# Kernel optimization log

Hardware: AMD Instinct MI355X
Metric: run time of the kernel (lower is better)

Reference implementation:

```python
import jax, jax.numpy as jnp
import numpy as np

B, D, K, A = 32768, 256, 1024, 32
MIN_LOG_STD, MAX_LOG_STD = -20.0, 2.0


def setup_inputs() -> dict:
    key = jax.random.key(0)
    ks = jax.random.split(key, 9)
    return {
        "obs": jax.random.normal(ks[0], (B, D), dtype=jnp.float32),
        "mean_C": jax.random.normal(ks[1], (K, D), dtype=jnp.float32),
        "mean_sigma": jnp.abs(jax.random.normal(ks[2], (K,), dtype=jnp.float32)) + 0.1,
        "mean_w": jax.random.normal(ks[3], (A, K), dtype=jnp.float32),
        "mean_b": jax.random.normal(ks[4], (A,), dtype=jnp.float32),
        "std_C": jax.random.normal(ks[5], (K, D), dtype=jnp.float32),
        "std_sigma": jnp.abs(jax.random.normal(ks[6], (K,), dtype=jnp.float32)) + 0.1,
        "std_w": jax.random.normal(ks[7], (A, K), dtype=jnp.float32),
        "std_b": jax.random.normal(ks[8], (A,), dtype=jnp.float32),
    }


def _rbf(x, C, sigma_sq, w, b):
    # r[b,k] = sum_d (x[b,d] - C[k,d])^2, expanded to avoid a [B,K,D] intermediate
    x2 = jnp.sum(x * x, axis=-1, keepdims=True)           # [B,1]
    c2 = jnp.sum(C * C, axis=-1)[None, :]                  # [1,K]
    r = x2 - 2.0 * (x @ C.T) + c2                          # [B,K]
    phi = jnp.exp(-r / (2.0 * jnp.abs(sigma_sq)[None, :]))  # [B,K]
    return phi @ w.T + b[None, :]                          # [B,A]


def reference(obs, mean_C, mean_sigma, mean_w, mean_b,
              std_C, std_sigma, std_w, std_b):
    action_mean = _rbf(obs, mean_C, mean_sigma, mean_w, mean_b)
    std_raw = _rbf(obs, std_C, std_sigma, std_w, std_b)
    action_std = jnp.exp(jnp.clip(std_raw, MIN_LOG_STD, MAX_LOG_STD))
    return jnp.concatenate((action_mean, action_std), axis=-1)  # [B, 2A]
```

## Files before the change

kernel.cpp:

```cpp
#include <hip/hip_runtime.h>


typedef float floatx4 __attribute__((ext_vector_type(4)));
typedef int   intx4  __attribute__((ext_vector_type(4)));
typedef unsigned int u32;
typedef unsigned char u8;

constexpr float LOG2E = 1.4426950408889634f;
constexpr float QS    = 25.4f;
constexpr float SINV2 = (5.0f / 127.0f) * (5.0f / 127.0f);

__device__ __forceinline__ u32 pk_fp8(float a, float b, float c, float d) {
  u32 v = __builtin_amdgcn_cvt_pk_fp8_f32(a, b, 0u, 0);
  v = __builtin_amdgcn_cvt_pk_fp8_f32(c, d, v, 1);
  return v;
}
__device__ __forceinline__ long mk64(u32 lo, u32 hi) {
  return (long)lo | ((long)hi << 32);
}
__device__ __forceinline__ int q8(float x) {
  return (int)rintf(fminf(fmaxf(x * QS, -127.f), 127.f));
}
__device__ __forceinline__ u32 pk_i8(int a, int b, int c, int d) {
  return (u32)(a & 255) | ((u32)(b & 255) << 8) | ((u32)(c & 255) << 16) | ((u32)(d & 255) << 24);
}

__global__ void prep(const float* __restrict__ mC, const float* __restrict__ mS,
                     const float* __restrict__ sC, const float* __restrict__ sS,
                     const float* __restrict__ mw, const float* __restrict__ sw,
                     u8* __restrict__ Cb2, float* __restrict__ a2g,
                     float* __restrict__ g2n, u8* __restrict__ wt)
{
  const int blk = blockIdx.x;
  if (blk < 512) {
    const int wq = threadIdx.x >> 6;
    const int t  = threadIdx.x & 63;
    const int b  = blk * 4 + wq;
    const int half = b >> 10;
    const int k = b & 1023;
    const float* src = (half ? sC : mC) + (size_t)k * 256;
    float4 f = *(const float4*)(src + t * 4);
    int i0 = q8(f.x), i1 = q8(f.y), i2 = q8(f.z), i3 = q8(f.w);
    const int ct = b >> 6, row = b & 63;
    const int wvv = row >> 4, cc = row & 15;
    const int ks = t >> 4, qq = (t >> 2) & 3, j0 = (t & 3) * 4;
    *(u32*)(Cb2 + (size_t)ct * 16384 + wvv * 4096 + (ks * 64 + qq * 16 + cc) * 16 + j0) =
        pk_i8(i0, i1, i2, i3);
    int is = i0 * i0 + i1 * i1 + i2 * i2 + i3 * i3;
    for (int off = 32; off > 0; off >>= 1) is += __shfl_down(is, off, 64);
    if (t == 0) {
      float sig = fabsf((half ? sS : mS)[k]);
      float t2 = SINV2 * LOG2E * 0.5f / sig;
      a2g[b] = 2.f * t2;
      g2n[b] = -t2 * (float)is;
    }
  } else {
    const int m   = blk - 512;
    const int tid = threadIdx.x;
    const int wv  = tid >> 6;
    const int lane = tid & 63;
    const int c   = lane & 15;
    const int q   = lane >> 4;
    const int kbE = ((2 * m) & 15) * 64 + 16 * wv + 4 * q;
    const float* src = (m < 8) ? mw : sw;
    float4 f00 = *(const float4*)(src + (size_t)c * 1024 + kbE);
    float4 f01 = *(const float4*)(src + (size_t)c * 1024 + kbE + 64);
    float4 f10 = *(const float4*)(src + (size_t)(16 + c) * 1024 + kbE);
    float4 f11 = *(const float4*)(src + (size_t)(16 + c) * 1024 + kbE + 64);
    uint4 o;
    o.x = pk_fp8(f00.x, f00.y, f00.z, f00.w);
    o.y = pk_fp8(f01.x, f01.y, f01.z, f01.w);
    o.z = pk_fp8(f10.x, f10.y, f10.z, f10.w);
    o.w = pk_fp8(f11.x, f11.y, f11.z, f11.w);
    *(uint4*)(wt + ((size_t)m * 256 + tid) * 16) = o;
  }
}

__global__ __launch_bounds__(256, 2)
void policy_main(const float* __restrict__ obs,
                 const u8* __restrict__ Cb2,
                 const float* __restrict__ a2g,
                 const float* __restrict__ g2n,
                 const u8* __restrict__ wt,
                 const float* __restrict__ mbias,
                 const float* __restrict__ sbias,
                 float* __restrict__ out)
{
  __shared__ __align__(16) char smem[69888];
  float* x2p = (float*)(smem + 16384);
  float* red = (float*)smem;

  const int tid  = threadIdx.x;
  const int lane = tid & 63;
  const int wv   = tid >> 6;
  const int c    = lane & 15;
  const int q    = lane >> 4;
  const int row0 = blockIdx.x * 64;
  const int kslc = 16 * wv + 4 * q;
  const int cfo  = wv * 4096 + lane * 16;
  const u8* wtl  = wt + (size_t)tid * 16;

#define LOADCF(CF, t)                                                     \
  { const u8* g0_ = Cb2 + (size_t)(t) * 16384 + cfo;                      \
    CF[0] = *(const intx4*)(g0_);                                         \
    CF[1] = *(const intx4*)(g0_ + 1024);                                  \
    CF[2] = *(const intx4*)(g0_ + 2048);                                  \
    CF[3] = *(const intx4*)(g0_ + 3072); }

  intx4 cfU[4], cfV[4];
  LOADCF(cfU, 0)
  LOADCF(cfV, 1)

  #pragma unroll
  for (int i = 0; i < 4; ++i) {
    int s = i * 256 + tid;
    int row = s >> 4;
    int s16 = s & 15;
    int l16 = s16 ^ (row & 15);
    const float* src = obs + (size_t)(row0 + row) * 256 + l16 * 16;
    float4 f0 = ((const float4*)src)[0];
    float4 f1 = ((const float4*)src)[1];
    float4 f2 = ((const float4*)src)[2];
    float4 f3 = ((const float4*)src)[3];
    int a0 = q8(f0.x), a1v = q8(f0.y), a2v = q8(f0.z), a3 = q8(f0.w);
    int b0 = q8(f1.x), b1 = q8(f1.y), b2 = q8(f1.z), b3 = q8(f1.w);
    int c0 = q8(f2.x), c1 = q8(f2.y), c2 = q8(f2.z), c3 = q8(f2.w);
    int d0 = q8(f3.x), d1 = q8(f3.y), d2 = q8(f3.z), d3 = q8(f3.w);
    uint4 pk;
    pk.x = pk_i8(a0, a1v, a2v, a3);
    pk.y = pk_i8(b0, b1, b2, b3);
    pk.z = pk_i8(c0, c1, c2, c3);
    pk.w = pk_i8(d0, d1, d2, d3);
    *(uint4*)(smem + s * 16) = pk;
    int is = a0*a0 + a1v*a1v + a2v*a2v + a3*a3
           + b0*b0 + b1*b1 + b2*b2 + b3*b3
           + c0*c0 + c1*c1 + c2*c2 + c3*c3
           + d0*d0 + d1*d1 + d2*d2 + d3*d3;
    x2p[row * 16 + s16] = (float)is;
  }
  __syncthreads();

  intx4 ob[4][4];
  #pragma unroll
  for (int nt = 0; nt < 4; ++nt) {
    const int row = nt * 16 + c;
    #pragma unroll
    for (int ks = 0; ks < 4; ++ks) {
      int slot = (4 * ks + q) ^ (row & 15);
      ob[nt][ks] = *(const intx4*)(smem + row * 256 + slot * 16);
    }
  }
  if (tid < 64) {
    float s = 0.f;
    #pragma unroll
    for (int j = 0; j < 16; j += 4) {
      float4 a = *(const float4*)(x2p + tid * 16 + j);
      s += a.x + a.y + a.z + a.w;
    }
    x2p[1024 + tid] = s;
  }
  __syncthreads();

  float hx2[4];
  #pragma unroll
  for (int nt = 0; nt < 4; ++nt) hx2[nt] = 0.5f * x2p[1024 + nt * 16 + c];

  const intx4 Z4i = {0, 0, 0, 0};
  const floatx4 Z4 = {0.f, 0.f, 0.f, 0.f};
  floatx4 acc2m[2][4], acc2s[2][4];
  #pragma unroll
  for (int a2i = 0; a2i < 2; ++a2i)
    #pragma unroll
    for (int nt = 0; nt < 4; ++nt) {
      acc2m[a2i][nt] = Z4;
      acc2s[a2i][nt] = Z4;
    }

  intx4 a1E[4], a1O[4];
  u32 pE[4], pc[4];

#define GEMM1PAIR()                                                             \
  { _Pragma("unroll")                                                           \
    for (int nt = 0; nt < 4; ++nt) {                                            \
      a1E[nt] = __builtin_amdgcn_mfma_i32_16x16x64_i8(cfU[0], ob[nt][0], Z4i, 0, 0, 0); \
      a1O[nt] = __builtin_amdgcn_mfma_i32_16x16x64_i8(cfV[0], ob[nt][0], Z4i, 0, 0, 0); \
    }                                                                           \
    _Pragma("unroll")                                                           \
    for (int ks = 1; ks < 4; ++ks) {                                            \
      _Pragma("unroll")                                                         \
      for (int nt = 0; nt < 4; ++nt) {                                          \
        a1E[nt] = __builtin_amdgcn_mfma_i32_16x16x64_i8(cfU[ks], ob[nt][ks], a1E[nt], 0, 0, 0); \
        a1O[nt] = __builtin_amdgcn_mfma_i32_16x16x64_i8(cfV[ks], ob[nt][ks], a1O[nt], 0, 0, 0); \
      }                                                                         \
    } }

#define EXPP(A1, AC, GC, DST)                                                   \
  { _Pragma("unroll")                                                           \
    for (int nt = 0; nt < 4; ++nt) {                                            \
      float t0 = (float)A1[nt][0] - hx2[nt], t1 = (float)A1[nt][1] - hx2[nt];   \
      float t2 = (float)A1[nt][2] - hx2[nt], t3 = (float)A1[nt][3] - hx2[nt];   \
      DST[nt] = pk_fp8(__builtin_amdgcn_exp2f(fmaf(AC.x, t0, GC.x)),            \
                       __builtin_amdgcn_exp2f(fmaf(AC.y, t1, GC.y)),            \
                       __builtin_amdgcn_exp2f(fmaf(AC.z, t2, GC.z)),            \
                       __builtin_amdgcn_exp2f(fmaf(AC.w, t3, GC.w))); } }

#define GEMM2P(ACC, WV4)                                                        \
  { long wA0 = mk64(WV4.x, WV4.y), wA1 = mk64(WV4.z, WV4.w);                    \
    _Pragma("unroll")                                                           \
    for (int nt = 0; nt < 4; ++nt) {                                            \
      long pb = mk64(pE[nt], pc[nt]);                                           \
      ACC[0][nt] = __builtin_amdgcn_mfma_f32_16x16x32_fp8_fp8(wA0, pb, ACC[0][nt], 0, 0, 0); \
      ACC[1][nt] = __builtin_amdgcn_mfma_f32_16x16x32_fp8_fp8(wA1, pb, ACC[1][nt], 0, 0, 0); \
    } }

#define STEP(m, ACC, PF)                                                        \
  {                                                                             \
    const int e = 2 * (m);                                                      \
    uint4 wv4 = *(const uint4*)(wtl + (size_t)(m) * 4096);                      \
    float4 acE = *(const float4*)(a2g + e * 64 + kslc);                         \
    float4 gcE = *(const float4*)(g2n + e * 64 + kslc);                         \
    float4 acO = *(const float4*)(a2g + (e + 1) * 64 + kslc);                   \
    float4 gcO = *(const float4*)(g2n + (e + 1) * 64 + kslc);                   \
    GEMM1PAIR()                                                                 \
    if (PF) { LOADCF(cfU, e + 2) LOADCF(cfV, e + 3) }                           \
    EXPP(a1E, acE, gcE, pE)                                                     \
    EXPP(a1O, acO, gcO, pc)                                                     \
    GEMM2P(ACC, wv4)                                                            \
  }

  #pragma unroll
  for (int m = 0; m < 8; ++m) STEP(m, acc2m, 1)
  #pragma unroll
  for (int m = 8; m < 15; ++m) STEP(m, acc2s, 1)
  STEP(15, acc2s, 0)
#undef STEP
#undef GEMM1PAIR
#undef EXPP
#undef GEMM2P
#undef LOADCF

  {
    float* myr = red + wv * 4352;
    #pragma unroll
    for (int a2i = 0; a2i < 2; ++a2i)
      #pragma unroll
      for (int nt = 0; nt < 4; ++nt) {
        *(floatx4*)(myr + (nt * 16 + c) * 68 + a2i * 16 + 4 * q)      = acc2m[a2i][nt];
        *(floatx4*)(myr + (nt * 16 + c) * 68 + 32 + a2i * 16 + 4 * q) = acc2s[a2i][nt];
      }
  }
  __syncthreads();

  #pragma unroll
  for (int i = 0; i < 16; ++i) {
    int idx = tid + 256 * i;
    int a = idx & 63;
    int b = idx >> 6;
    float v = red[b * 68 + a] + red[4352 + b * 68 + a] +
              red[8704 + b * 68 + a] + red[13056 + b * 68 + a];
    if (a < 32) {
      v += mbias[a];
    } else {
      v += sbias[a - 32];
      v = fminf(fmaxf(v, -20.f), 2.f);
      v = __builtin_amdgcn_exp2f(v * LOG2E);
    }
    out[(size_t)(row0 + b) * 64 + a] = v;
  }
}

extern "C" void kernel_launch(void* const* d_in, const int* in_sizes, int n_in,
                              void* d_out, int out_size, void* d_ws, size_t ws_size,
                              hipStream_t stream) {
  const float* obs = (const float*)d_in[0];
  const float* mC  = (const float*)d_in[1];
  const float* mS  = (const float*)d_in[2];
  const float* mW  = (const float*)d_in[3];
  const float* mB  = (const float*)d_in[4];
  const float* sC  = (const float*)d_in[5];
  const float* sS  = (const float*)d_in[6];
  const float* sW  = (const float*)d_in[7];
  const float* sB  = (const float*)d_in[8];
  float* out = (float*)d_out;

  u8*    Cb2 = (u8*)d_ws;
  float* a2g = (float*)((char*)d_ws + 2048 * 256);
  float* g2n = a2g + 2048;
  u8*    wt  = (u8*)(g2n + 2048);

  prep<<<528, 256, 0, stream>>>(mC, mS, sC, sS, mW, sW, Cb2, a2g, g2n, wt);
  policy_main<<<512, 256, 0, stream>>>(obs, Cb2, a2g, g2n, wt, mB, sB, out);
}
```

Baseline: 116.9 us.

## Split work per block into 32 rows and one RBF head for higher occupancy

Each block now handles 32 rows and only one of the two RBF heads (mean or std), chosen by the block index. The grid grows from 512 to 2048 blocks and shared memory shrinks from about 68KB to 18KB, with launch bounds raised to 8 blocks per CU. Register and LDS pressure drop and the GPU gets more parallel blocks to cover latency. In exchange, each obs row is loaded and quantized twice, once per head, and C-matrix fetches are amortized over fewer rows per block.

```diff
diff --git a/kernel.cpp b/kernel.cpp
--- a/kernel.cpp
+++ b/kernel.cpp
@@ -76,7 +76,7 @@
   }
 }
 
-__global__ __launch_bounds__(256, 2)
+__global__ __launch_bounds__(256, 8)
 void policy_main(const float* __restrict__ obs,
                  const u8* __restrict__ Cb2,
                  const float* __restrict__ a2g,
@@ -86,8 +86,8 @@
                  const float* __restrict__ sbias,
                  float* __restrict__ out)
 {
-  __shared__ __align__(16) char smem[69888];
-  float* x2p = (float*)(smem + 16384);
+  __shared__ __align__(16) char smem[18432];
+  float* x2p = (float*)(smem + 8192);
   float* red = (float*)smem;
 
   const int tid  = threadIdx.x;
@@ -95,13 +95,18 @@
   const int wv   = tid >> 6;
   const int c    = lane & 15;
   const int q    = lane >> 4;
-  const int row0 = blockIdx.x * 64;
+  const int half = blockIdx.x & 1;
+  const int row0 = (blockIdx.x >> 1) * 32;
   const int kslc = 16 * wv + 4 * q;
   const int cfo  = wv * 4096 + lane * 16;
-  const u8* wtl  = wt + (size_t)tid * 16;
+
+  const u8*    cbh = Cb2 + (size_t)half * (16 * 16384);
+  const float* a2h = a2g + half * 1024;
+  const float* g2h = g2n + half * 1024;
+  const u8*    wtl = wt + (size_t)half * 32768 + (size_t)tid * 16;
 
 #define LOADCF(CF, t)                                                     \
-  { const u8* g0_ = Cb2 + (size_t)(t) * 16384 + cfo;                      \
+  { const u8* g0_ = cbh + (size_t)(t) * 16384 + cfo;                      \
     CF[0] = *(const intx4*)(g0_);                                         \
     CF[1] = *(const intx4*)(g0_ + 1024);                                  \
     CF[2] = *(const intx4*)(g0_ + 2048);                                  \
@@ -112,7 +117,7 @@
   LOADCF(cfV, 1)
 
   #pragma unroll
-  for (int i = 0; i < 4; ++i) {
+  for (int i = 0; i < 2; ++i) {
     int s = i * 256 + tid;
     int row = s >> 4;
     int s16 = s & 15;
@@ -140,9 +145,9 @@
   }
   __syncthreads();
 
-  intx4 ob[4][4];
-  #pragma unroll
-  for (int nt = 0; nt < 4; ++nt) {
+  intx4 ob[2][4];
+  #pragma unroll
+  for (int nt = 0; nt < 2; ++nt) {
     const int row = nt * 16 + c;
     #pragma unroll
     for (int ks = 0; ks < 4; ++ks) {
@@ -150,45 +155,42 @@
       ob[nt][ks] = *(const intx4*)(smem + row * 256 + slot * 16);
     }
   }
-  if (tid < 64) {
-    float s = 0.f;
+  if (tid < 32) {
+    float ssum = 0.f;
     #pragma unroll
     for (int j = 0; j < 16; j += 4) {
       float4 a = *(const float4*)(x2p + tid * 16 + j);
-      s += a.x + a.y + a.z + a.w;
-    }
-    x2p[1024 + tid] = s;
-  }
-  __syncthreads();
-
-  float hx2[4];
-  #pragma unroll
-  for (int nt = 0; nt < 4; ++nt) hx2[nt] = 0.5f * x2p[1024 + nt * 16 + c];
+      ssum += a.x + a.y + a.z + a.w;
+    }
+    x2p[512 + tid] = ssum;
+  }
+  __syncthreads();
+
+  float hx2[2];
+  hx2[0] = 0.5f * x2p[512 + c];
+  hx2[1] = 0.5f * x2p[512 + 16 + c];
 
   const intx4 Z4i = {0, 0, 0, 0};
   const floatx4 Z4 = {0.f, 0.f, 0.f, 0.f};
-  floatx4 acc2m[2][4], acc2s[2][4];
+  floatx4 acc[2][2];
   #pragma unroll
   for (int a2i = 0; a2i < 2; ++a2i)
     #pragma unroll
-    for (int nt = 0; nt < 4; ++nt) {
-      acc2m[a2i][nt] = Z4;
-      acc2s[a2i][nt] = Z4;
-    }
-
-  intx4 a1E[4], a1O[4];
-  u32 pE[4], pc[4];
+    for (int nt = 0; nt < 2; ++nt) acc[a2i][nt] = Z4;
+
+  intx4 a1E[2], a1O[2];
+  u32 pE[2], pc[2];
 
 #define GEMM1PAIR()                                                             \
   { _Pragma("unroll")                                                           \
-    for (int nt = 0; nt < 4; ++nt) {                                            \
+    for (int nt = 0; nt < 2; ++nt) {                                            \
       a1E[nt] = __builtin_amdgcn_mfma_i32_16x16x64_i8(cfU[0], ob[nt][0], Z4i, 0, 0, 0); \
       a1O[nt] = __builtin_amdgcn_mfma_i32_16x16x64_i8(cfV[0], ob[nt][0], Z4i, 0, 0, 0); \
     }                                                                           \
     _Pragma("unroll")                                                           \
     for (int ks = 1; ks < 4; ++ks) {                                            \
       _Pragma("unroll")                                                         \
-      for (int nt = 0; nt < 4; ++nt) {                                          \
+      for (int nt = 0; nt < 2; ++nt) {                                          \
         a1E[nt] = __builtin_amdgcn_mfma_i32_16x16x64_i8(cfU[ks], ob[nt][ks], a1E[nt], 0, 0, 0); \
         a1O[nt] = __builtin_amdgcn_mfma_i32_16x16x64_i8(cfV[ks], ob[nt][ks], a1O[nt], 0, 0, 0); \
       }                                                                         \
@@ -196,7 +198,7 @@
 
 #define EXPP(A1, AC, GC, DST)                                                   \
   { _Pragma("unroll")                                                           \
-    for (int nt = 0; nt < 4; ++nt) {                                            \
+    for (int nt = 0; nt < 2; ++nt) {                                            \
       float t0 = (float)A1[nt][0] - hx2[nt], t1 = (float)A1[nt][1] - hx2[nt];   \
       float t2 = (float)A1[nt][2] - hx2[nt], t3 = (float)A1[nt][3] - hx2[nt];   \
       DST[nt] = pk_fp8(__builtin_amdgcn_exp2f(fmaf(AC.x, t0, GC.x)),            \
@@ -204,68 +206,63 @@
                        __builtin_amdgcn_exp2f(fmaf(AC.z, t2, GC.z)),            \
                        __builtin_amdgcn_exp2f(fmaf(AC.w, t3, GC.w))); } }
 
-#define GEMM2P(ACC, WV4)                                                        \
+#define GEMM2P(WV4)                                                             \
   { long wA0 = mk64(WV4.x, WV4.y), wA1 = mk64(WV4.z, WV4.w);                    \
     _Pragma("unroll")                                                           \
-    for (int nt = 0; nt < 4; ++nt) {                                            \
+    for (int nt = 0; nt < 2; ++nt) {                                            \
       long pb = mk64(pE[nt], pc[nt]);                                           \
-      ACC[0][nt] = __builtin_amdgcn_mfma_f32_16x16x32_fp8_fp8(wA0, pb, ACC[0][nt], 0, 0, 0); \
-      ACC[1][nt] = __builtin_amdgcn_mfma_f32_16x16x32_fp8_fp8(wA1, pb, ACC[1][nt], 0, 0, 0); \
+      acc[0][nt] = __builtin_amdgcn_mfma_f32_16x16x32_fp8_fp8(wA0, pb, acc[0][nt], 0, 0, 0); \
+      acc[1][nt] = __builtin_amdgcn_mfma_f32_16x16x32_fp8_fp8(wA1, pb, acc[1][nt], 0, 0, 0); \
     } }
 
-#define STEP(m, ACC, PF)                                                        \
+#define STEP(mm, PF)                                                            \
   {                                                                             \
-    const int e = 2 * (m);                                                      \
-    uint4 wv4 = *(const uint4*)(wtl + (size_t)(m) * 4096);                      \
-    float4 acE = *(const float4*)(a2g + e * 64 + kslc);                         \
-    float4 gcE = *(const float4*)(g2n + e * 64 + kslc);                         \
-    float4 acO = *(const float4*)(a2g + (e + 1) * 64 + kslc);                   \
-    float4 gcO = *(const float4*)(g2n + (e + 1) * 64 + kslc);                   \
+    uint4 wv4 = *(const uint4*)(wtl + (size_t)(mm) * 4096);                     \
+    float4 acE = *(const float4*)(a2h + (2 * (mm)) * 64 + kslc);                \
+    float4 gcE = *(const float4*)(g2h + (2 * (mm)) * 64 + kslc);                \
+    float4 acO = *(const float4*)(a2h + (2 * (mm) + 1) * 64 + kslc);            \
+    float4 gcO = *(const float4*)(g2h + (2 * (mm) + 1) * 64 + kslc);            \
     GEMM1PAIR()                                                                 \
-    if (PF) { LOADCF(cfU, e + 2) LOADCF(cfV, e + 3) }                           \
+    if (PF) { LOADCF(cfU, 2 * (mm) + 2) LOADCF(cfV, 2 * (mm) + 3) }             \
     EXPP(a1E, acE, gcE, pE)                                                     \
     EXPP(a1O, acO, gcO, pc)                                                     \
-    GEMM2P(ACC, wv4)                                                            \
-  }
-
-  #pragma unroll
-  for (int m = 0; m < 8; ++m) STEP(m, acc2m, 1)
-  #pragma unroll
-  for (int m = 8; m < 15; ++m) STEP(m, acc2s, 1)
-  STEP(15, acc2s, 0)
+    GEMM2P(wv4)                                                                 \
+  }
+
+  #pragma unroll
+  for (int mm = 0; mm < 7; ++mm) STEP(mm, 1)
+  STEP(7, 0)
 #undef STEP
 #undef GEMM1PAIR
 #undef EXPP
 #undef GEMM2P
 #undef LOADCF
 
+  __syncthreads();
   {
-    float* myr = red + wv * 4352;
+    float* myr = red + wv * 1152;
     #pragma unroll
     for (int a2i = 0; a2i < 2; ++a2i)
       #pragma unroll
-      for (int nt = 0; nt < 4; ++nt) {
-        *(floatx4*)(myr + (nt * 16 + c) * 68 + a2i * 16 + 4 * q)      = acc2m[a2i][nt];
-        *(floatx4*)(myr + (nt * 16 + c) * 68 + 32 + a2i * 16 + 4 * q) = acc2s[a2i][nt];
-      }
-  }
-  __syncthreads();
-
-  #pragma unroll
-  for (int i = 0; i < 16; ++i) {
+      for (int nt = 0; nt < 2; ++nt)
+        *(floatx4*)(myr + (nt * 16 + c) * 36 + a2i * 16 + 4 * q) = acc[a2i][nt];
+  }
+  __syncthreads();
+
+  const float* bias = half ? sbias : mbias;
+  #pragma unroll
+  for (int i = 0; i < 4; ++i) {
     int idx = tid + 256 * i;
-    int a = idx & 63;
-    int b = idx >> 6;
-    float v = red[b * 68 + a] + red[4352 + b * 68 + a] +
-              red[8704 + b * 68 + a] + red[13056 + b * 68 + a];
-    if (a < 32) {
-      v += mbias[a];
-    } else {
-      v += sbias[a - 32];
+    int a = idx & 31;
+    int b = idx >> 5;
+    float v = red[b * 36 + a] + red[1152 + b * 36 + a] +
+              red[2304 + b * 36 + a] + red[3456 + b * 36 + a];
+    v += bias[a];
+    if (half) {
       v = fminf(fmaxf(v, -20.f), 2.f);
       v = __builtin_amdgcn_exp2f(v * LOG2E);
     }
-    out[(size_t)(row0 + b) * 64 + a] = v;
+    out[(size_t)(row0 + b) * 64 + half * 32 + a] = v;
   }
 }
 
@@ -289,5 +286,5 @@
   u8*    wt  = (u8*)(g2n + 2048);
 
   prep<<<528, 256, 0, stream>>>(mC, mS, sC, sS, mW, sW, Cb2, a2g, g2n, wt);
-  policy_main<<<512, 256, 0, stream>>>(obs, Cb2, a2g, g2n, wt, mB, sB, out);
-}
+  policy_main<<<2048, 256, 0, stream>>>(obs, Cb2, a2g, g2n, wt, mB, sB, out);
+}
```

Measured after the change: 363.6 us. 211% more time.

## Software-pipeline GEMM1 one step ahead of exp and GEMM2

Applied to the files above, without the earlier changes.

Restructures the main loop so each iteration issues the next step's first-GEMM MFMAs and prefetches the next weights and coefficients before running the exp and second-GEMM on the previous step's saved results. The aim is to overlap MFMA latency with the transcendental exp work and hide load latency. The cost is extra live registers for the saved accumulators and prefetched operands, which could raise register pressure and lower occupancy.

```diff
diff --git a/kernel.cpp b/kernel.cpp
--- a/kernel.cpp
+++ b/kernel.cpp
@@ -213,27 +213,44 @@
       ACC[1][nt] = __builtin_amdgcn_mfma_f32_16x16x32_fp8_fp8(wA1, pb, ACC[1][nt], 0, 0, 0); \
     } }
 
-#define STEP(m, ACC, PF)                                                        \
-  {                                                                             \
-    const int e = 2 * (m);                                                      \
-    uint4 wv4 = *(const uint4*)(wtl + (size_t)(m) * 4096);                      \
-    float4 acE = *(const float4*)(a2g + e * 64 + kslc);                         \
-    float4 gcE = *(const float4*)(g2n + e * 64 + kslc);                         \
-    float4 acO = *(const float4*)(a2g + (e + 1) * 64 + kslc);                   \
-    float4 gcO = *(const float4*)(g2n + (e + 1) * 64 + kslc);                   \
-    GEMM1PAIR()                                                                 \
-    if (PF) { LOADCF(cfU, e + 2) LOADCF(cfV, e + 3) }                           \
-    EXPP(a1E, acE, gcE, pE)                                                     \
-    EXPP(a1O, acO, gcO, pc)                                                     \
-    GEMM2P(ACC, wv4)                                                            \
-  }
-
-  #pragma unroll
-  for (int m = 0; m < 8; ++m) STEP(m, acc2m, 1)
-  #pragma unroll
-  for (int m = 8; m < 15; ++m) STEP(m, acc2s, 1)
-  STEP(15, acc2s, 0)
-#undef STEP
+  uint4  wv4c = *(const uint4*)(wtl);
+  float4 acEc = *(const float4*)(a2g + kslc);
+  float4 gcEc = *(const float4*)(g2n + kslc);
+  float4 acOc = *(const float4*)(a2g + 64 + kslc);
+  float4 gcOc = *(const float4*)(g2n + 64 + kslc);
+
+  GEMM1PAIR()
+  LOADCF(cfU, 2) LOADCF(cfV, 3)
+
+  #pragma unroll
+  for (int mm = 0; mm < 16; ++mm) {
+    intx4 s1E[4], s1O[4];
+    #pragma unroll
+    for (int nt = 0; nt < 4; ++nt) { s1E[nt] = a1E[nt]; s1O[nt] = a1O[nt]; }
+
+    uint4  wv4n = wv4c;
+    float4 acEn = acEc, gcEn = gcEc, acOn = acOc, gcOn = gcOc;
+    if (mm < 15) {
+      wv4n = *(const uint4*)(wtl + (size_t)(mm + 1) * 4096);
+      acEn = *(const float4*)(a2g + (2 * (mm + 1)) * 64 + kslc);
+      gcEn = *(const float4*)(g2n + (2 * (mm + 1)) * 64 + kslc);
+      acOn = *(const float4*)(a2g + (2 * (mm + 1) + 1) * 64 + kslc);
+      gcOn = *(const float4*)(g2n + (2 * (mm + 1) + 1) * 64 + kslc);
+    }
+
+    if (mm < 15) {
+      GEMM1PAIR()
+    }
+    if (mm < 14) {
+      LOADCF(cfU, 2 * (mm + 2)) LOADCF(cfV, 2 * (mm + 2) + 1)
+    }
+
+    EXPP(s1E, acEc, gcEc, pE)
+    EXPP(s1O, acOc, gcOc, pc)
+    if (mm < 8) { GEMM2P(acc2m, wv4c) } else { GEMM2P(acc2s, wv4c) }
+
+    wv4c = wv4n; acEc = acEn; gcEc = gcEn; acOc = acOn; gcOc = gcOn;
+  }
 #undef GEMM1PAIR
 #undef EXPP
 #undef GEMM2P
```

After: 117.3 us. About the same (+0.3%).
